# Kernel optimization log

Measured on AMD Instinct MI355X. Metric: run time of the kernel, lower is better.

## Reference

```python
import jax, jax.numpy as jnp
import numpy as np

N_NODES = 50000
N_EDGES = 1600000
H_DIM = 128
OUT_DIM = 128
N_RELS = 16


def setup_inputs() -> dict:
    key = jax.random.key(0)
    k1, k2, k3, k4, k5, k6 = jax.random.split(key, 6)
    node_ids = jnp.arange(N_NODES, dtype=jnp.int64) if jax.config.jax_enable_x64 else jnp.arange(N_NODES, dtype=jnp.int32)
    src = jax.random.randint(k1, (N_EDGES,), 0, N_NODES, dtype=jnp.int32)
    dst = jax.random.randint(k2, (N_EDGES,), 0, N_NODES, dtype=jnp.int32)
    rel = jax.random.randint(k3, (N_EDGES,), 0, N_RELS, dtype=jnp.int32)
    norm = jax.random.uniform(k4, (N_EDGES, 1), dtype=jnp.float32)
    emb_table = jax.random.normal(k5, (N_NODES, H_DIM), dtype=jnp.float32)
    W = jax.random.normal(k6, (N_RELS, H_DIM, OUT_DIM), dtype=jnp.float32) * (1.0 / np.sqrt(H_DIM))
    return {"node_ids": node_ids, "src": src, "dst": dst, "rel": rel,
            "norm": norm, "emb_table": emb_table, "W": W}


def reference(node_ids, src, dst, rel, norm, emb_table, W):
    # Input layer: embedding lookup on node ids.  [N, h_dim]
    h = emb_table[node_ids]
    n_nodes = emb_table.shape[0]
    # RelGraphConv (full per-relation weight, no basis, no self-loop,
    # activation=None for the single/last layer, dropout inactive at eval):
    # Transform all node features by every relation weight up front
    # (R small, avoids [E, d, o] per-edge weight gather).  [R, N, out]
    h_rel = jnp.einsum('nd,rdo->rno', h, W)
    # Gather per-edge transformed source features, apply edge norm.  [E, out]
    msg = h_rel[rel, src] * norm
    # Scatter-sum messages to destination nodes.  [N, out]
    out = jax.ops.segment_sum(msg, dst, num_segments=n_nodes)
    return out
```

## Files before the change

### kernel.cpp

```cpp
#include <hip/hip_runtime.h>
#include <hip/hip_bf16.h>

#define NN 50000
#define NE 1600000
#define HD 128
#define NR 16
#define NCB 1563
#define S2B 512
#define EPB (NE / S2B)
#define SLOT 2048
#define TOTSLOT 3200000
#define PREPH_BLKS 6250
#define PREPW_BLKS 1024

typedef __bf16 bf16x8 __attribute__((ext_vector_type(8)));
typedef unsigned short u16x8 __attribute__((ext_vector_type(8)));
typedef float f32x4 __attribute__((ext_vector_type(4)));

__device__ __forceinline__ unsigned short f2bf(float f) {
    union { float f; unsigned int u; } v; v.f = f;
    unsigned int u = v.u;
    u += 0x7FFFu + ((u >> 16) & 1u);
    return (unsigned short)(u >> 16);
}
__device__ __forceinline__ float bflo(unsigned int u) {
    union { unsigned int u; float f; } v; v.u = u << 16; return v.f;
}
__device__ __forceinline__ float bfhi(unsigned int u) {
    union { unsigned int u; float f; } v; v.u = u & 0xFFFF0000u; return v.f;
}

__global__ __launch_bounds__(256) void prep_all(const int* __restrict__ node_ids,
                                                const float* __restrict__ emb,
                                                unsigned short* __restrict__ h_bf,
                                                const float* __restrict__ W,
                                                unsigned short* __restrict__ Wt,
                                                const int* __restrict__ dst,
                                                int* __restrict__ cntM) {
    const int b = blockIdx.x;
    const int t = threadIdx.x;
    if (b < PREPH_BLKS) {
        int gid = b * 256 + t;
        int row = gid >> 5;
        int c = (gid & 31) << 2;
        int nid = node_ids[row];
        if (nid < 0) nid = 0; if (nid >= NN) nid = NN - 1;
        float4 v = *(const float4*)(emb + (size_t)nid * HD + c);
        ushort4 o;
        o.x = f2bf(v.x); o.y = f2bf(v.y); o.z = f2bf(v.z); o.w = f2bf(v.w);
        *(ushort4*)(h_bf + (size_t)row * HD + c) = o;
    } else if (b < PREPH_BLKS + PREPW_BLKS) {
        int gid = (b - PREPH_BLKS) * 256 + t;
        int r = gid >> 14;
        int idx = gid & 16383;
        int k = idx >> 7;
        int o = idx & 127;
        Wt[(size_t)r * 16384 + (size_t)o * 128 + k] = f2bf(W[gid]);
    } else {
        __shared__ int h[NCB];
        const int sb = b - PREPH_BLKS - PREPW_BLKS;
        for (int i = t; i < NCB; i += 256) h[i] = 0;
        __syncthreads();
        const int base = sb * EPB;
        for (int i = t; i < EPB; i += 256)
            atomicAdd(&h[((unsigned)dst[base + i]) >> 5], 1);
        __syncthreads();
        for (int i = t; i < NCB; i += 256) cntM[sb * NCB + i] = h[i];
    }
}

__global__ __launch_bounds__(256) void scanBins(int* __restrict__ cntM,
                                                int* __restrict__ binN) {
    __shared__ int s[256];
    const int t = threadIdx.x;
    const int bin = blockIdx.x;
    int v0 = cntM[(2 * t) * NCB + bin];
    int v1 = cntM[(2 * t + 1) * NCB + bin];
    s[t] = v0 + v1;
    __syncthreads();
    for (int off = 1; off < 256; off <<= 1) {
        int x = (t >= off) ? s[t - off] : 0;
        __syncthreads();
        s[t] += x;
        __syncthreads();
    }
    int total = s[255];
    int e0 = s[t] - v0 - v1;
    int e1 = e0 + v0;
    int cap = (bin == NCB - 1) ? (TOTSLOT - (NCB - 1) * SLOT) : SLOT;
    cntM[(2 * t) * NCB + bin]     = bin * SLOT + (e0 < cap ? e0 : cap);
    cntM[(2 * t + 1) * NCB + bin] = bin * SLOT + (e1 < cap ? e1 : cap);
    if (t == 255) binN[bin] = (total < cap) ? total : cap;
}

__global__ __launch_bounds__(256) void s2_scatter(const int* __restrict__ src,
                                                  const int* __restrict__ dst,
                                                  const int* __restrict__ rel,
                                                  const float* __restrict__ norm,
                                                  const int* __restrict__ cntM,
                                                  uint2* __restrict__ recs) {
    __shared__ int cur[NCB];
    const int t = threadIdx.x, sb = blockIdx.x;
    for (int i = t; i < NCB; i += 256) cur[i] = cntM[sb * NCB + i];
    __syncthreads();
    const int base = sb * EPB;
    for (int i = t; i < EPB; i += 256) {
        int e = base + i;
        int d = dst[e];
        int bin = ((unsigned)d) >> 5;
        int p = atomicAdd(&cur[bin], 1);
        int binEnd = (bin == NCB - 1) ? TOTSLOT : (bin + 1) * SLOT;
        if (p < binEnd) {
            unsigned x = (unsigned)src[e] | ((unsigned)rel[e] << 16)
                       | ((unsigned)(d & 31) << 20);
            recs[p] = make_uint2(x, __float_as_uint(norm[e]));
        }
    }
}

__global__ __launch_bounds__(256) void gemm_hrel(const unsigned short* __restrict__ h_bf,
                                                 const unsigned short* __restrict__ Wt,
                                                 unsigned short* __restrict__ h_rel) {
    __shared__ unsigned short sA[128][136];
    __shared__ unsigned short sB[128][136];
    const int t = threadIdx.x;
    const int base = blockIdx.x * 128;
    const int rg = blockIdx.y;

    #pragma unroll
    for (int j = 0; j < 8; ++j) {
        int idx = t + j * 256;
        int row = idx >> 4;
        int c8 = (idx & 15) << 3;
        int g = base + row;
        if (g >= NN) g = 0;
        uint4 v = *(const uint4*)(h_bf + (size_t)g * 128 + c8);
        *(uint4*)&sA[row][c8] = v;
    }

    const int lane = t & 63;
    const int w = t >> 6;
    const int wr = w >> 1, wc = w & 1;
    const int l15 = lane & 15, lhi = lane >> 4;

    for (int rr = 0; rr < 4; ++rr) {
        const int r = rg * 4 + rr;
        if (rr > 0) __syncthreads();
        const unsigned short* wp = Wt + ((size_t)r << 14);
        #pragma unroll
        for (int j = 0; j < 8; ++j) {
            int idx = t + j * 256;
            int row = idx >> 4;
            int c8 = (idx & 15) << 3;
            uint4 v = *(const uint4*)(wp + (size_t)row * 128 + c8);
            *(uint4*)&sB[row][c8] = v;
        }
        __syncthreads();

        f32x4 acc[4][4];
        #pragma unroll
        for (int i = 0; i < 4; ++i)
            #pragma unroll
            for (int j = 0; j < 4; ++j)
                acc[i][j] = (f32x4){0.f, 0.f, 0.f, 0.f};

        #pragma unroll
        for (int kt = 0; kt < 4; ++kt) {
            const int ko = kt * 32 + lhi * 8;
            bf16x8 aF[4], bF[4];
            #pragma unroll
            for (int ms = 0; ms < 4; ++ms) {
                u16x8 raw = *(const u16x8*)&sA[wr * 64 + ms * 16 + l15][ko];
                aF[ms] = __builtin_bit_cast(bf16x8, raw);
            }
            #pragma unroll
            for (int nt = 0; nt < 4; ++nt) {
                u16x8 raw = *(const u16x8*)&sB[wc * 64 + nt * 16 + l15][ko];
                bF[nt] = __builtin_bit_cast(bf16x8, raw);
            }
            #pragma unroll
            for (int ms = 0; ms < 4; ++ms)
                #pragma unroll
                for (int nt = 0; nt < 4; ++nt)
                    acc[ms][nt] = __builtin_amdgcn_mfma_f32_16x16x32_bf16(
                        aF[ms], bF[nt], acc[ms][nt], 0, 0, 0);
        }

        __syncthreads();
        #pragma unroll
        for (int ms = 0; ms < 4; ++ms)
            #pragma unroll
            for (int nt = 0; nt < 4; ++nt)
                #pragma unroll
                for (int reg = 0; reg < 4; ++reg)
                    sB[wr * 64 + ms * 16 + lhi * 4 + reg]
                      [wc * 64 + nt * 16 + l15] = f2bf(acc[ms][nt][reg]);
        __syncthreads();
        size_t rbase = ((size_t)r * NN + base) * 128;
        #pragma unroll
        for (int j = 0; j < 8; ++j) {
            int idx = t + j * 256;
            int row = idx >> 4;
            int c8 = (idx & 15) << 3;
            if (base + row < NN) {
                uint4 v = *(const uint4*)&sB[row][c8];
                *(uint4*)(h_rel + rbase + (size_t)row * 128 + c8) = v;
            }
        }
    }
}

__global__ __launch_bounds__(256) void seg_fused(const int* __restrict__ binN,
                                                 const uint2* __restrict__ recs,
                                                 const unsigned int* __restrict__ hb,
                                                 float* __restrict__ out) {
    __shared__ uint2 rec[SLOT];
    __shared__ unsigned char sub8[SLOT];
    __shared__ unsigned short idx16[SLOT];
    __shared__ int h[32], sbx[33], cur[32];
    const int t = threadIdx.x;
    const int bin = blockIdx.x;
    const int n = binN[bin];
    const uint2* rg = recs + (size_t)bin * SLOT;

    if (t < 32) h[t] = 0;
    __syncthreads();
    for (int i = t; i < n; i += 256) {
        uint2 r = rg[i];
        int sub = (r.x >> 20) & 31;
        rec[i] = make_uint2(((r.x >> 16) & 15) * (unsigned)NN + (r.x & 0xFFFFu),
                            r.y);
        sub8[i] = (unsigned char)sub;
        atomicAdd(&h[sub], 1);
    }
    __syncthreads();
    if (t == 0) {
        int run = 0;
        #pragma unroll
        for (int s = 0; s < 32; ++s) { sbx[s] = run; run += h[s]; }
        sbx[32] = run;
    }
    __syncthreads();
    if (t < 32) cur[t] = sbx[t];
    __syncthreads();
    for (int i = t; i < n; i += 256) {
        int p = atomicAdd(&cur[sub8[i]], 1);
        idx16[p] = (unsigned short)i;
    }
    __syncthreads();

    const int lane = t & 63;
    const int w = t >> 6;
    #pragma unroll
    for (int k = 0; k < 8; ++k) {
        int j = w * 8 + k;
        int d = bin * 32 + j;
        if (d >= NN) continue;
        int beg = sbx[j], end = sbx[j + 1];
        float a0 = 0.f, a1 = 0.f;
        int i = beg;
        for (; i + 7 < end; i += 8) {
            int i0 = idx16[i],     i1 = idx16[i + 1];
            int i2 = idx16[i + 2], i3 = idx16[i + 3];
            int i4 = idx16[i + 4], i5 = idx16[i + 5];
            int i6 = idx16[i + 6], i7 = idx16[i + 7];
            uint2 r0 = rec[i0], r1 = rec[i1], r2 = rec[i2], r3 = rec[i3];
            uint2 r4 = rec[i4], r5 = rec[i5], r6 = rec[i6], r7 = rec[i7];
            unsigned u0 = hb[r0.x * 64u + lane];
            unsigned u1 = hb[r1.x * 64u + lane];
            unsigned u2 = hb[r2.x * 64u + lane];
            unsigned u3 = hb[r3.x * 64u + lane];
            unsigned u4 = hb[r4.x * 64u + lane];
            unsigned u5 = hb[r5.x * 64u + lane];
            unsigned u6 = hb[r6.x * 64u + lane];
            unsigned u7 = hb[r7.x * 64u + lane];
            float n0 = __uint_as_float(r0.y), n1 = __uint_as_float(r1.y);
            float n2 = __uint_as_float(r2.y), n3 = __uint_as_float(r3.y);
            float n4 = __uint_as_float(r4.y), n5 = __uint_as_float(r5.y);
            float n6 = __uint_as_float(r6.y), n7 = __uint_as_float(r7.y);
            a0 += bflo(u0) * n0 + bflo(u1) * n1 + bflo(u2) * n2 + bflo(u3) * n3;
            a1 += bfhi(u0) * n0 + bfhi(u1) * n1 + bfhi(u2) * n2 + bfhi(u3) * n3;
            a0 += bflo(u4) * n4 + bflo(u5) * n5 + bflo(u6) * n6 + bflo(u7) * n7;
            a1 += bfhi(u4) * n4 + bfhi(u5) * n5 + bfhi(u6) * n6 + bfhi(u7) * n7;
        }
        for (; i < end; ++i) {
            uint2 rc = rec[idx16[i]];
            unsigned u = hb[rc.x * 64u + lane];
            float nm = __uint_as_float(rc.y);
            a0 += bflo(u) * nm;
            a1 += bfhi(u) * nm;
        }
        *(float2*)(out + (size_t)d * 128 + lane * 2) = make_float2(a0, a1);
    }
}


extern "C" void kernel_launch(void* const* d_in, const int* in_sizes, int n_in,
                              void* d_out, int out_size, void* d_ws, size_t ws_size,
                              hipStream_t stream) {
    const int* node_ids = (const int*)d_in[0];
    const int* src      = (const int*)d_in[1];
    const int* dst      = (const int*)d_in[2];
    const int* rel      = (const int*)d_in[3];
    const float* norm   = (const float*)d_in[4];
    const float* emb    = (const float*)d_in[5];
    const float* W      = (const float*)d_in[6];
    float* out = (float*)d_out;

    char* ws = (char*)d_ws;
    unsigned short* h_rel = (unsigned short*)(ws);
    unsigned short* h_bf  = (unsigned short*)(ws + 204800000);
    unsigned short* Wt    = (unsigned short*)(ws + 217600000);
    int* cntM             = (int*)(ws + 218124288);
    int* binN             = (int*)(ws + 221325312);

    uint2* recs = (uint2*)d_out;

    prep_all<<<PREPH_BLKS + PREPW_BLKS + S2B, 256, 0, stream>>>(
        node_ids, emb, h_bf, W, Wt, dst, cntM);
    scanBins<<<NCB, 256, 0, stream>>>(cntM, binN);
    s2_scatter<<<S2B, 256, 0, stream>>>(src, dst, rel, norm, cntM, recs);
    gemm_hrel<<<dim3(391, 4), 256, 0, stream>>>(h_bf, Wt, h_rel);
    seg_fused<<<NCB, 256, 0, stream>>>(binN, recs,
                                       (const unsigned int*)h_rel, out);
}
```

Measured before the change: 300.8 us.

## Aggregate raw embeddings per relation then apply W via MFMA in fused kernel

Reorders the computation from transform-then-gather to gather-then-transform. Each destination bin first sums normalized source embeddings per (relation, destination), then multiplies the 32x128 per-relation aggregate by W_r with MFMA, accumulating across all 16 relations. This removes the large h_rel GEMM and its roughly 200MB intermediate write and read, and gathers come from the much smaller bf16 embedding table. In exchange, the aggregates are rounded to bf16 before the matmul, the gather loop is split into 16 relation passes with load-imbalanced inner loops, and W is read from global memory in every block.

Result: slower. 372.9 us (+24.0%).

```diff
diff --git a/kernel.cpp b/kernel.cpp
--- a/kernel.cpp
+++ b/kernel.cpp
@@ -9,7 +9,7 @@
 #define S2B 512
 #define EPB (NE / S2B)
 #define SLOT 2048
-#define TOTSLOT 3200000
+#define NB 512
 #define PREPH_BLKS 6250
 #define PREPW_BLKS 1024
 
@@ -87,10 +87,9 @@
     int total = s[255];
     int e0 = s[t] - v0 - v1;
     int e1 = e0 + v0;
-    int cap = (bin == NCB - 1) ? (TOTSLOT - (NCB - 1) * SLOT) : SLOT;
-    cntM[(2 * t) * NCB + bin]     = bin * SLOT + (e0 < cap ? e0 : cap);
-    cntM[(2 * t + 1) * NCB + bin] = bin * SLOT + (e1 < cap ? e1 : cap);
-    if (t == 255) binN[bin] = (total < cap) ? total : cap;
+    cntM[(2 * t) * NCB + bin]     = bin * SLOT + (e0 < SLOT ? e0 : SLOT);
+    cntM[(2 * t + 1) * NCB + bin] = bin * SLOT + (e1 < SLOT ? e1 : SLOT);
+    if (t == 255) binN[bin] = (total < SLOT) ? total : SLOT;
 }
 
 __global__ __launch_bounds__(256) void s2_scatter(const int* __restrict__ src,
@@ -109,7 +108,7 @@
         int d = dst[e];
         int bin = ((unsigned)d) >> 5;
         int p = atomicAdd(&cur[bin], 1);
-        int binEnd = (bin == NCB - 1) ? TOTSLOT : (bin + 1) * SLOT;
+        int binEnd = (bin + 1) * SLOT;
         if (p < binEnd) {
             unsigned x = (unsigned)src[e] | ((unsigned)rel[e] << 16)
                        | ((unsigned)(d & 31) << 20);
@@ -118,179 +117,138 @@
     }
 }
 
-__global__ __launch_bounds__(256) void gemm_hrel(const unsigned short* __restrict__ h_bf,
-                                                 const unsigned short* __restrict__ Wt,
-                                                 unsigned short* __restrict__ h_rel) {
-    __shared__ unsigned short sA[128][136];
-    __shared__ unsigned short sB[128][136];
-    const int t = threadIdx.x;
-    const int base = blockIdx.x * 128;
-    const int rg = blockIdx.y;
-
-    #pragma unroll
-    for (int j = 0; j < 8; ++j) {
-        int idx = t + j * 256;
-        int row = idx >> 4;
-        int c8 = (idx & 15) << 3;
-        int g = base + row;
-        if (g >= NN) g = 0;
-        uint4 v = *(const uint4*)(h_bf + (size_t)g * 128 + c8);
-        *(uint4*)&sA[row][c8] = v;
-    }
-
-    const int lane = t & 63;
-    const int w = t >> 6;
-    const int wr = w >> 1, wc = w & 1;
-    const int l15 = lane & 15, lhi = lane >> 4;
-
-    for (int rr = 0; rr < 4; ++rr) {
-        const int r = rg * 4 + rr;
-        if (rr > 0) __syncthreads();
-        const unsigned short* wp = Wt + ((size_t)r << 14);
-        #pragma unroll
-        for (int j = 0; j < 8; ++j) {
-            int idx = t + j * 256;
-            int row = idx >> 4;
-            int c8 = (idx & 15) << 3;
-            uint4 v = *(const uint4*)(wp + (size_t)row * 128 + c8);
-            *(uint4*)&sB[row][c8] = v;
-        }
-        __syncthreads();
-
-        f32x4 acc[4][4];
-        #pragma unroll
-        for (int i = 0; i < 4; ++i)
-            #pragma unroll
-            for (int j = 0; j < 4; ++j)
-                acc[i][j] = (f32x4){0.f, 0.f, 0.f, 0.f};
-
-        #pragma unroll
-        for (int kt = 0; kt < 4; ++kt) {
-            const int ko = kt * 32 + lhi * 8;
-            bf16x8 aF[4], bF[4];
-            #pragma unroll
-            for (int ms = 0; ms < 4; ++ms) {
-                u16x8 raw = *(const u16x8*)&sA[wr * 64 + ms * 16 + l15][ko];
-                aF[ms] = __builtin_bit_cast(bf16x8, raw);
-            }
-            #pragma unroll
-            for (int nt = 0; nt < 4; ++nt) {
-                u16x8 raw = *(const u16x8*)&sB[wc * 64 + nt * 16 + l15][ko];
-                bF[nt] = __builtin_bit_cast(bf16x8, raw);
-            }
-            #pragma unroll
-            for (int ms = 0; ms < 4; ++ms)
-                #pragma unroll
-                for (int nt = 0; nt < 4; ++nt)
-                    acc[ms][nt] = __builtin_amdgcn_mfma_f32_16x16x32_bf16(
-                        aF[ms], bF[nt], acc[ms][nt], 0, 0, 0);
-        }
-
-        __syncthreads();
-        #pragma unroll
-        for (int ms = 0; ms < 4; ++ms)
-            #pragma unroll
-            for (int nt = 0; nt < 4; ++nt)
-                #pragma unroll
-                for (int reg = 0; reg < 4; ++reg)
-                    sB[wr * 64 + ms * 16 + lhi * 4 + reg]
-                      [wc * 64 + nt * 16 + l15] = f2bf(acc[ms][nt][reg]);
-        __syncthreads();
-        size_t rbase = ((size_t)r * NN + base) * 128;
-        #pragma unroll
-        for (int j = 0; j < 8; ++j) {
-            int idx = t + j * 256;
-            int row = idx >> 4;
-            int c8 = (idx & 15) << 3;
-            if (base + row < NN) {
-                uint4 v = *(const uint4*)&sB[row][c8];
-                *(uint4*)(h_rel + rbase + (size_t)row * 128 + c8) = v;
-            }
-        }
-    }
-}
-
-__global__ __launch_bounds__(256) void seg_fused(const int* __restrict__ binN,
+__global__ __launch_bounds__(256, 4) void seg_mm(const int* __restrict__ binN,
                                                  const uint2* __restrict__ recs,
                                                  const unsigned int* __restrict__ hb,
+                                                 const unsigned short* __restrict__ Wt,
                                                  float* __restrict__ out) {
-    __shared__ uint2 rec[SLOT];
-    __shared__ unsigned char sub8[SLOT];
-    __shared__ unsigned short idx16[SLOT];
-    __shared__ int h[32], sbx[33], cur[32];
+    __shared__ int srcS[SLOT];
+    __shared__ float normS[SLOT];
+    __shared__ int h[NB];
+    __shared__ int sbx[NB + 1];
+    __shared__ int sc[256];
+    __shared__ __align__(16) unsigned m32[2][32][68];
     const int t = threadIdx.x;
     const int bin = blockIdx.x;
     const int n = binN[bin];
     const uint2* rg = recs + (size_t)bin * SLOT;
 
-    if (t < 32) h[t] = 0;
+    for (int i = t; i < NB; i += 256) h[i] = 0;
+    __syncthreads();
+    for (int i = t; i < n; i += 256) {
+        unsigned x = rg[i].x;
+        atomicAdd(&h[((x >> 16) & 15) * 32 + ((x >> 20) & 31)], 1);
+    }
+    __syncthreads();
+    int v0 = h[2 * t], v1 = h[2 * t + 1];
+    sc[t] = v0 + v1;
+    __syncthreads();
+    for (int off = 1; off < 256; off <<= 1) {
+        int x = (t >= off) ? sc[t - off] : 0;
+        __syncthreads();
+        sc[t] += x;
+        __syncthreads();
+    }
+    int e0 = sc[t] - v0 - v1;
+    sbx[2 * t] = e0;
+    sbx[2 * t + 1] = e0 + v0;
+    if (t == 255) sbx[NB] = sc[255];
+    h[2 * t] = e0;
+    h[2 * t + 1] = e0 + v0;
     __syncthreads();
     for (int i = t; i < n; i += 256) {
         uint2 r = rg[i];
-        int sub = (r.x >> 20) & 31;
-        rec[i] = make_uint2(((r.x >> 16) & 15) * (unsigned)NN + (r.x & 0xFFFFu),
-                            r.y);
-        sub8[i] = (unsigned char)sub;
-        atomicAdd(&h[sub], 1);
-    }
-    __syncthreads();
-    if (t == 0) {
-        int run = 0;
-        #pragma unroll
-        for (int s = 0; s < 32; ++s) { sbx[s] = run; run += h[s]; }
-        sbx[32] = run;
-    }
-    __syncthreads();
-    if (t < 32) cur[t] = sbx[t];
-    __syncthreads();
-    for (int i = t; i < n; i += 256) {
-        int p = atomicAdd(&cur[sub8[i]], 1);
-        idx16[p] = (unsigned short)i;
+        int key = ((r.x >> 16) & 15) * 32 + ((r.x >> 20) & 31);
+        int p = atomicAdd(&h[key], 1);
+        srcS[p] = r.x & 0xFFFF;
+        normS[p] = __uint_as_float(r.y);
     }
     __syncthreads();
 
     const int lane = t & 63;
     const int w = t >> 6;
+    const int l15 = lane & 15, lhi = lane >> 4;
+    const int colBase = w * 32;
+
+    f32x4 acc[2][2];
     #pragma unroll
-    for (int k = 0; k < 8; ++k) {
-        int j = w * 8 + k;
-        int d = bin * 32 + j;
-        if (d >= NN) continue;
-        int beg = sbx[j], end = sbx[j + 1];
-        float a0 = 0.f, a1 = 0.f;
-        int i = beg;
-        for (; i + 7 < end; i += 8) {
-            int i0 = idx16[i],     i1 = idx16[i + 1];
-            int i2 = idx16[i + 2], i3 = idx16[i + 3];
-            int i4 = idx16[i + 4], i5 = idx16[i + 5];
-            int i6 = idx16[i + 6], i7 = idx16[i + 7];
-            uint2 r0 = rec[i0], r1 = rec[i1], r2 = rec[i2], r3 = rec[i3];
-            uint2 r4 = rec[i4], r5 = rec[i5], r6 = rec[i6], r7 = rec[i7];
-            unsigned u0 = hb[r0.x * 64u + lane];
-            unsigned u1 = hb[r1.x * 64u + lane];
-            unsigned u2 = hb[r2.x * 64u + lane];
-            unsigned u3 = hb[r3.x * 64u + lane];
-            unsigned u4 = hb[r4.x * 64u + lane];
-            unsigned u5 = hb[r5.x * 64u + lane];
-            unsigned u6 = hb[r6.x * 64u + lane];
-            unsigned u7 = hb[r7.x * 64u + lane];
-            float n0 = __uint_as_float(r0.y), n1 = __uint_as_float(r1.y);
-            float n2 = __uint_as_float(r2.y), n3 = __uint_as_float(r3.y);
-            float n4 = __uint_as_float(r4.y), n5 = __uint_as_float(r5.y);
-            float n6 = __uint_as_float(r6.y), n7 = __uint_as_float(r7.y);
-            a0 += bflo(u0) * n0 + bflo(u1) * n1 + bflo(u2) * n2 + bflo(u3) * n3;
-            a1 += bfhi(u0) * n0 + bfhi(u1) * n1 + bfhi(u2) * n2 + bfhi(u3) * n3;
-            a0 += bflo(u4) * n4 + bflo(u5) * n5 + bflo(u6) * n6 + bflo(u7) * n7;
-            a1 += bfhi(u4) * n4 + bfhi(u5) * n5 + bfhi(u6) * n6 + bfhi(u7) * n7;
-        }
-        for (; i < end; ++i) {
-            uint2 rc = rec[idx16[i]];
-            unsigned u = hb[rc.x * 64u + lane];
-            float nm = __uint_as_float(rc.y);
-            a0 += bflo(u) * nm;
-            a1 += bfhi(u) * nm;
-        }
-        *(float2*)(out + (size_t)d * 128 + lane * 2) = make_float2(a0, a1);
+    for (int i = 0; i < 2; ++i)
+        #pragma unroll
+        for (int j = 0; j < 2; ++j)
+            acc[i][j] = (f32x4){0.f, 0.f, 0.f, 0.f};
+
+    for (int r = 0; r < NR; ++r) {
+        const int p = r & 1;
+        int beg[8], end[8];
+        float A0[8], A1[8];
+        int mx = 0;
+        #pragma unroll
+        for (int k = 0; k < 8; ++k) {
+            beg[k] = sbx[r * 32 + w * 8 + k];
+            end[k] = sbx[r * 32 + w * 8 + k + 1];
+            A0[k] = 0.f; A1[k] = 0.f;
+            int len = end[k] - beg[k];
+            mx = len > mx ? len : mx;
+        }
+        for (int rd = 0; rd < mx; ++rd) {
+            unsigned u[8]; float nm[8];
+            #pragma unroll
+            for (int k = 0; k < 8; ++k) {
+                if (beg[k] + rd < end[k]) {
+                    int s = srcS[beg[k] + rd];
+                    nm[k] = normS[beg[k] + rd];
+                    u[k] = hb[((unsigned)s << 6) + lane];
+                }
+            }
+            #pragma unroll
+            for (int k = 0; k < 8; ++k) {
+                if (beg[k] + rd < end[k]) {
+                    A0[k] += bflo(u[k]) * nm[k];
+                    A1[k] += bfhi(u[k]) * nm[k];
+                }
+            }
+        }
+        #pragma unroll
+        for (int k = 0; k < 8; ++k)
+            m32[p][w * 8 + k][lane] =
+                ((unsigned)f2bf(A1[k]) << 16) | (unsigned)f2bf(A0[k]);
+        __syncthreads();
+        const unsigned short* wp = Wt + ((size_t)r << 14);
+        #pragma unroll
+        for (int kt = 0; kt < 4; ++kt) {
+            const int ko = kt * 32 + lhi * 8;
+            bf16x8 aF[2], bF[2];
+            #pragma unroll
+            for (int ms = 0; ms < 2; ++ms) {
+                u16x8 raw = *(const u16x8*)((const unsigned short*)&m32[p][ms * 16 + l15][0] + ko);
+                aF[ms] = __builtin_bit_cast(bf16x8, raw);
+            }
+            #pragma unroll
+            for (int nt = 0; nt < 2; ++nt) {
+                u16x8 raw = *(const u16x8*)(wp + (size_t)(colBase + nt * 16 + l15) * 128 + ko);
+                bF[nt] = __builtin_bit_cast(bf16x8, raw);
+            }
+            #pragma unroll
+            for (int ms = 0; ms < 2; ++ms)
+                #pragma unroll
+                for (int nt = 0; nt < 2; ++nt)
+                    acc[ms][nt] = __builtin_amdgcn_mfma_f32_16x16x32_bf16(
+                        aF[ms], bF[nt], acc[ms][nt], 0, 0, 0);
+        }
+    }
+
+    const int dbase = bin * 32;
+    #pragma unroll
+    for (int ms = 0; ms < 2; ++ms) {
+        #pragma unroll
+        for (int reg = 0; reg < 4; ++reg) {
+            int d = dbase + ms * 16 + lhi * 4 + reg;
+            if (d < NN) {
+                #pragma unroll
+                for (int nt = 0; nt < 2; ++nt)
+                    out[(size_t)d * 128 + colBase + nt * 16 + l15] = acc[ms][nt][reg];
+            }
+        }
     }
 }
 
@@ -308,19 +266,16 @@
     float* out = (float*)d_out;
 
     char* ws = (char*)d_ws;
-    unsigned short* h_rel = (unsigned short*)(ws);
-    unsigned short* h_bf  = (unsigned short*)(ws + 204800000);
-    unsigned short* Wt    = (unsigned short*)(ws + 217600000);
-    int* cntM             = (int*)(ws + 218124288);
-    int* binN             = (int*)(ws + 221325312);
-
-    uint2* recs = (uint2*)d_out;
+    unsigned short* h_bf = (unsigned short*)(ws);
+    unsigned short* Wt   = (unsigned short*)(ws + 12800000);
+    int* cntM            = (int*)(ws + 13324288);
+    int* binN            = (int*)(ws + 16525312);
+    uint2* recs          = (uint2*)(ws + 16531712);
 
     prep_all<<<PREPH_BLKS + PREPW_BLKS + S2B, 256, 0, stream>>>(
         node_ids, emb, h_bf, W, Wt, dst, cntM);
     scanBins<<<NCB, 256, 0, stream>>>(cntM, binN);
     s2_scatter<<<S2B, 256, 0, stream>>>(src, dst, rel, norm, cntM, recs);
-    gemm_hrel<<<dim3(391, 4), 256, 0, stream>>>(h_bf, Wt, h_rel);
-    seg_fused<<<NCB, 256, 0, stream>>>(binN, recs,
-                                       (const unsigned int*)h_rel, out);
-}
+    seg_mm<<<NCB, 256, 0, stream>>>(binN, recs,
+                                    (const unsigned int*)h_bf, Wt, out);
+}
```

## Replace count-scan-scatter binning with sliced fixed-capacity global atomic bucketing

Applied to the files above, without the earlier changes.

Removes the per-block histogram pass and the bin scan kernel. Edges are now bucketed directly with global atomics into 16 fixed-capacity slices per destination bin. The consumer compacts the slices using the per-slice counters. This saves one kernel launch and a read pass over dst, at the cost of contended global atomics and silently dropping edges if any slice overflows its capacity of 128.

Result: slower. 351.3 us (+16.8%).

```diff
diff --git a/kernel.cpp b/kernel.cpp
--- a/kernel.cpp
+++ b/kernel.cpp
@@ -6,12 +6,12 @@
 #define HD 128
 #define NR 16
 #define NCB 1563
-#define S2B 512
-#define EPB (NE / S2B)
+#define NSL 16
+#define SCAP 128
 #define SLOT 2048
-#define TOTSLOT 3200000
 #define PREPH_BLKS 6250
 #define PREPW_BLKS 1024
+#define SCAT_BLKS 6250
 
 typedef __bf16 bf16x8 __attribute__((ext_vector_type(8)));
 typedef unsigned short u16x8 __attribute__((ext_vector_type(8)));
@@ -35,8 +35,7 @@
                                                 unsigned short* __restrict__ h_bf,
                                                 const float* __restrict__ W,
                                                 unsigned short* __restrict__ Wt,
-                                                const int* __restrict__ dst,
-                                                int* __restrict__ cntM) {
+                                                int* __restrict__ gcur) {
     const int b = blockIdx.x;
     const int t = threadIdx.x;
     if (b < PREPH_BLKS) {
@@ -57,64 +56,28 @@
         int o = idx & 127;
         Wt[(size_t)r * 16384 + (size_t)o * 128 + k] = f2bf(W[gid]);
     } else {
-        __shared__ int h[NCB];
-        const int sb = b - PREPH_BLKS - PREPW_BLKS;
-        for (int i = t; i < NCB; i += 256) h[i] = 0;
-        __syncthreads();
-        const int base = sb * EPB;
-        for (int i = t; i < EPB; i += 256)
-            atomicAdd(&h[((unsigned)dst[base + i]) >> 5], 1);
-        __syncthreads();
-        for (int i = t; i < NCB; i += 256) cntM[sb * NCB + i] = h[i];
-    }
-}
-
-__global__ __launch_bounds__(256) void scanBins(int* __restrict__ cntM,
-                                                int* __restrict__ binN) {
-    __shared__ int s[256];
-    const int t = threadIdx.x;
-    const int bin = blockIdx.x;
-    int v0 = cntM[(2 * t) * NCB + bin];
-    int v1 = cntM[(2 * t + 1) * NCB + bin];
-    s[t] = v0 + v1;
-    __syncthreads();
-    for (int off = 1; off < 256; off <<= 1) {
-        int x = (t >= off) ? s[t - off] : 0;
-        __syncthreads();
-        s[t] += x;
-        __syncthreads();
-    }
-    int total = s[255];
-    int e0 = s[t] - v0 - v1;
-    int e1 = e0 + v0;
-    int cap = (bin == NCB - 1) ? (TOTSLOT - (NCB - 1) * SLOT) : SLOT;
-    cntM[(2 * t) * NCB + bin]     = bin * SLOT + (e0 < cap ? e0 : cap);
-    cntM[(2 * t + 1) * NCB + bin] = bin * SLOT + (e1 < cap ? e1 : cap);
-    if (t == 255) binN[bin] = (total < cap) ? total : cap;
-}
-
-__global__ __launch_bounds__(256) void s2_scatter(const int* __restrict__ src,
-                                                  const int* __restrict__ dst,
-                                                  const int* __restrict__ rel,
-                                                  const float* __restrict__ norm,
-                                                  const int* __restrict__ cntM,
-                                                  uint2* __restrict__ recs) {
-    __shared__ int cur[NCB];
-    const int t = threadIdx.x, sb = blockIdx.x;
-    for (int i = t; i < NCB; i += 256) cur[i] = cntM[sb * NCB + i];
-    __syncthreads();
-    const int base = sb * EPB;
-    for (int i = t; i < EPB; i += 256) {
-        int e = base + i;
-        int d = dst[e];
-        int bin = ((unsigned)d) >> 5;
-        int p = atomicAdd(&cur[bin], 1);
-        int binEnd = (bin == NCB - 1) ? TOTSLOT : (bin + 1) * SLOT;
-        if (p < binEnd) {
-            unsigned x = (unsigned)src[e] | ((unsigned)rel[e] << 16)
-                       | ((unsigned)(d & 31) << 20);
-            recs[p] = make_uint2(x, __float_as_uint(norm[e]));
-        }
+        for (int i = t; i < NCB * NSL; i += 256) gcur[i] = 0;
+    }
+}
+
+__global__ __launch_bounds__(256) void scat(const int* __restrict__ src,
+                                            const int* __restrict__ dst,
+                                            const int* __restrict__ rel,
+                                            const float* __restrict__ norm,
+                                            int* __restrict__ gcur,
+                                            uint2* __restrict__ recs) {
+    int e = blockIdx.x * 256 + threadIdx.x;
+    if (e >= NE) return;
+    int slice = blockIdx.x & (NSL - 1);
+    int d = dst[e];
+    int bin = ((unsigned)d) >> 5;
+    int cap = (bin == NCB - 1) ? 64 : SCAP;
+    int p = atomicAdd(&gcur[bin * NSL + slice], 1);
+    if (p < cap) {
+        unsigned x = (unsigned)src[e] | ((unsigned)rel[e] << 16)
+                   | ((unsigned)(d & 31) << 20);
+        recs[(size_t)bin * SLOT + slice * cap + p] =
+            make_uint2(x, __float_as_uint(norm[e]));
     }
 }
 
@@ -210,7 +173,7 @@
     }
 }
 
-__global__ __launch_bounds__(256) void seg_fused(const int* __restrict__ binN,
+__global__ __launch_bounds__(256) void seg_fused(const int* __restrict__ gcur,
                                                  const uint2* __restrict__ recs,
                                                  const unsigned int* __restrict__ hb,
                                                  float* __restrict__ out) {
@@ -218,22 +181,39 @@
     __shared__ unsigned char sub8[SLOT];
     __shared__ unsigned short idx16[SLOT];
     __shared__ int h[32], sbx[33], cur[32];
+    __shared__ int c16[NSL], soff[NSL], nTot;
     const int t = threadIdx.x;
     const int bin = blockIdx.x;
-    const int n = binN[bin];
+    const int scap = (bin == NCB - 1) ? 64 : SCAP;
     const uint2* rg = recs + (size_t)bin * SLOT;
 
     if (t < 32) h[t] = 0;
-    __syncthreads();
-    for (int i = t; i < n; i += 256) {
-        uint2 r = rg[i];
-        int sub = (r.x >> 20) & 31;
-        rec[i] = make_uint2(((r.x >> 16) & 15) * (unsigned)NN + (r.x & 0xFFFFu),
-                            r.y);
-        sub8[i] = (unsigned char)sub;
-        atomicAdd(&h[sub], 1);
-    }
-    __syncthreads();
+    if (t < NSL) {
+        int c = gcur[bin * NSL + t];
+        c16[t] = c > scap ? scap : c;
+    }
+    __syncthreads();
+    if (t == 0) {
+        int run = 0;
+        #pragma unroll
+        for (int s = 0; s < NSL; ++s) { soff[s] = run; run += c16[s]; }
+        nTot = run;
+    }
+    __syncthreads();
+    #pragma unroll
+    for (int s = 0; s < NSL; ++s) {
+        if (t < c16[s]) {
+            uint2 r = rg[s * scap + t];
+            int i = soff[s] + t;
+            int sub = (r.x >> 20) & 31;
+            rec[i] = make_uint2(((r.x >> 16) & 15) * (unsigned)NN + (r.x & 0xFFFFu),
+                                r.y);
+            sub8[i] = (unsigned char)sub;
+            atomicAdd(&h[sub], 1);
+        }
+    }
+    __syncthreads();
+    const int n = nTot;
     if (t == 0) {
         int run = 0;
         #pragma unroll
@@ -311,16 +291,14 @@
     unsigned short* h_rel = (unsigned short*)(ws);
     unsigned short* h_bf  = (unsigned short*)(ws + 204800000);
     unsigned short* Wt    = (unsigned short*)(ws + 217600000);
-    int* cntM             = (int*)(ws + 218124288);
-    int* binN             = (int*)(ws + 221325312);
+    int* gcur             = (int*)(ws + 218124288);
 
     uint2* recs = (uint2*)d_out;
 
-    prep_all<<<PREPH_BLKS + PREPW_BLKS + S2B, 256, 0, stream>>>(
-        node_ids, emb, h_bf, W, Wt, dst, cntM);
-    scanBins<<<NCB, 256, 0, stream>>>(cntM, binN);
-    s2_scatter<<<S2B, 256, 0, stream>>>(src, dst, rel, norm, cntM, recs);
+    prep_all<<<PREPH_BLKS + PREPW_BLKS + 1, 256, 0, stream>>>(
+        node_ids, emb, h_bf, W, Wt, gcur);
+    scat<<<SCAT_BLKS, 256, 0, stream>>>(src, dst, rel, norm, gcur, recs);
     gemm_hrel<<<dim3(391, 4), 256, 0, stream>>>(h_bf, Wt, h_rel);
-    seg_fused<<<NCB, 256, 0, stream>>>(binN, recs,
+    seg_fused<<<NCB, 256, 0, stream>>>(gcur, recs,
                                        (const unsigned int*)h_rel, out);
 }
```
